# Kernel tuning notes

Measured on AMD Instinct MI355X. Metric: run time of the kernel, lower is better.

Reference implementation:

```python
import jax, jax.numpy as jnp
import numpy as np

N_ENT = 500000   # entity vocab
N_REL = 500      # relation vocab
D = 128          # embed_size
H = 256          # hidden_size
B = 4096         # number of support pairs
NBR = 32         # neighbors per node
NODES = 2 * B
T = NODES * NBR  # total neighbor edges


def setup_inputs() -> dict:
    key = jax.random.key(0)
    ks = jax.random.split(key, 12)
    entities = jax.random.randint(ks[0], (NODES,), 0, N_ENT)
    neighbor_entities = jax.random.randint(ks[1], (T,), 0, N_ENT)
    neighbor_relations = jax.random.randint(ks[2], (T,), 0, N_REL)
    offsets = (jnp.arange(NODES) * NBR).astype(jnp.int64 if jax.config.read('jax_enable_x64') else jnp.int32)
    def init(k, shape, fan_in):
        return jax.random.normal(k, shape, dtype=jnp.float32) * (1.0 / np.sqrt(fan_in))
    return dict(
        entity_embeddings=init(ks[3], (N_ENT, D), D),
        relation_embeddings=init(ks[4], (N_REL, D), D),
        Wt=init(ks[5], (D, H), D),      bt=jnp.zeros((H,), jnp.float32),
        Wn=init(ks[6], (2 * D, H), 2 * D), bn=jnp.zeros((H,), jnp.float32),
        Wr=init(ks[7], (2 * H, H), 2 * H), br=jnp.zeros((H,), jnp.float32),
        entities=entities,
        neighbor_entities=neighbor_entities,
        neighbor_relations=neighbor_relations,
        offsets=offsets,
    )


def _segment_mean(table, idx, offsets, num_segments):
    # embedding_bag(mode='mean') with ragged offsets
    n = idx.shape[0]
    seg = jnp.searchsorted(offsets, jnp.arange(n), side='right') - 1   # [T] bag id per edge
    counts = jnp.diff(jnp.concatenate([offsets, jnp.array([n], offsets.dtype)]))
    summed = jax.ops.segment_sum(table[idx], seg, num_segments=num_segments)
    return summed / jnp.maximum(counts, 1).astype(table.dtype)[:, None]


def reference(entity_embeddings, relation_embeddings, Wt, bt, Wn, bn, Wr, br,
              entities, neighbor_entities, neighbor_relations, offsets):
    nodes = entities.shape[0]
    # self-entity transform
    ent = entity_embeddings[entities] @ Wt + bt                        # [2B, H]
    # neighbor mean-aggregation (entity + relation bags share offsets)
    ne = _segment_mean(entity_embeddings, neighbor_entities, offsets, nodes)    # [2B, D]
    nr = _segment_mean(relation_embeddings, neighbor_relations, offsets, nodes)  # [2B, D]
    nbr = jnp.concatenate([ne, nr], axis=-1) @ Wn + bn                 # [2B, H]
    node = jax.nn.relu(ent + nbr).reshape(nodes // 2, 2 * Wt.shape[1])  # [B, 2H]
    pair = jax.nn.relu(node @ Wr + br)                                 # [B, H]
    return pair
```

## Files before the change

### kernel.cpp

```cpp
#include <hip/hip_runtime.h>
#include <hip/hip_bf16.h>

#define N_ENT   500000
#define N_REL   500
#define D       128
#define H       256
#define NPAIR   4096
#define NBR     32
#define NODES   8192
#define T_EDGES 262144
#define K1      384
#define K2      512

typedef __bf16  bf16x8  __attribute__((ext_vector_type(8)));
typedef float   floatx4 __attribute__((ext_vector_type(4)));

__device__ inline unsigned short f2bf(float f) {
  unsigned u = __float_as_uint(f);
  unsigned r = (u + 0x7fffu + ((u >> 16) & 1u)) >> 16;
  return (unsigned short)r;
}

__global__ __launch_bounds__(256) void gather_kernel(
    const float* __restrict__ ent_emb, const float* __restrict__ rel_emb,
    const int* __restrict__ entities, const int* __restrict__ nbr_ent,
    const int* __restrict__ nbr_rel, const int* __restrict__ offsets,
    unsigned short* __restrict__ X)
{
  int wave = threadIdx.x >> 6;
  int lane = threadIdx.x & 63;
  int n = blockIdx.x * 4 + wave;

  int beg = offsets[n];
  int end = (n + 1 < NODES) ? offsets[n + 1] : T_EDGES;
  int cnt = end - beg;

  const float2* ent2 = (const float2*)ent_emb;
  const float2* rel2 = (const float2*)rel_emb;

  int self = entities[n];
  float2 s = ent2[(long)self * 64 + lane];

  float sex = 0.f, sey = 0.f, srx = 0.f, sry = 0.f;

  if (cnt == NBR) {
    int ie[NBR], ir[NBR];
    #pragma unroll
    for (int k = 0; k < NBR; ++k) ie[k] = nbr_ent[beg + k];
    #pragma unroll
    for (int k = 0; k < NBR; ++k) ir[k] = nbr_rel[beg + k];

    #pragma unroll
    for (int c = 0; c < NBR / 8; ++c) {
      float2 e[8], r[8];
      #pragma unroll
      for (int j = 0; j < 8; ++j) e[j] = ent2[(long)ie[c * 8 + j] * 64 + lane];
      #pragma unroll
      for (int j = 0; j < 8; ++j) r[j] = rel2[(long)ir[c * 8 + j] * 64 + lane];
      #pragma unroll
      for (int j = 0; j < 8; ++j) {
        sex += e[j].x; sey += e[j].y;
        srx += r[j].x; sry += r[j].y;
      }
    }
  } else {
    for (int k = beg; k < end; ++k) {
      float2 e = ent2[(long)nbr_ent[k] * 64 + lane];
      float2 r = rel2[(long)nbr_rel[k] * 64 + lane];
      sex += e.x; sey += e.y; srx += r.x; sry += r.y;
    }
  }

  int cc = cnt < 1 ? 1 : cnt;
  float inv = 1.f / (float)cc;

  unsigned short* row = X + (long)n * K1;
  ushort2* p0 = (ushort2*)(row) + lane;
  ushort2* p1 = (ushort2*)(row + D) + lane;
  ushort2* p2 = (ushort2*)(row + 2 * D) + lane;
  *p0 = make_ushort2(f2bf(s.x), f2bf(s.y));
  *p1 = make_ushort2(f2bf(sex * inv), f2bf(sey * inv));
  *p2 = make_ushort2(f2bf(srx * inv), f2bf(sry * inv));
}

__global__ __launch_bounds__(256) void prep_weights(
    const float* __restrict__ Wt, const float* __restrict__ Wn,
    const float* __restrict__ Wr,
    unsigned short* __restrict__ W1t, unsigned short* __restrict__ W2t)
{
  int idx = blockIdx.x * 256 + threadIdx.x;
  if (idx < H * K1) {
    int nn = idx / K1, k = idx % K1;
    float v = (k < D) ? Wt[k * H + nn] : Wn[(k - D) * H + nn];
    W1t[idx] = f2bf(v);
  }
  if (idx < H * K2) {
    int nn = idx / K2, k = idx % K2;
    W2t[idx] = f2bf(Wr[k * H + nn]);
  }
}

template<int K>
__global__ __launch_bounds__(256) void gemm_bias_relu(
    const bf16x8* __restrict__ A8,
    const bf16x8* __restrict__ Bt8,
    const float* __restrict__ bias0, const float* __restrict__ bias1,
    unsigned short* __restrict__ out_bf, float* __restrict__ out_f, int N)
{
  constexpr int K8 = K / 8;
  __shared__ bf16x8 Ash[64 * 4];
  __shared__ bf16x8 Bsh[64 * 4];

  int tid  = threadIdx.x;
  int wave = tid >> 6, lane = tid & 63;
  int quad = lane >> 4, l15 = lane & 15;
  int bm = blockIdx.x * 64, bn = blockIdx.y * 64;
  int r  = tid >> 2;
  int s4 = tid & 3;

  floatx4 acc[4];
  #pragma unroll
  for (int i = 0; i < 4; ++i) acc[i] = (floatx4){0.f, 0.f, 0.f, 0.f};

  for (int k0 = 0; k0 < K8; k0 += 4) {
    Ash[tid] = A8[(long)(bm + r) * K8 + k0 + s4];
    Bsh[tid] = Bt8[(long)(bn + r) * K8 + k0 + s4];
    __syncthreads();
    bf16x8 a = Ash[(wave * 16 + l15) * 4 + quad];
    #pragma unroll
    for (int nt = 0; nt < 4; ++nt) {
      bf16x8 b = Bsh[(nt * 16 + l15) * 4 + quad];
      acc[nt] = __builtin_amdgcn_mfma_f32_16x16x32_bf16(a, b, acc[nt], 0, 0, 0);
    }
    __syncthreads();
  }

  #pragma unroll
  for (int nt = 0; nt < 4; ++nt) {
    int gn = bn + nt * 16 + l15;
    float bs = bias0[gn] + (bias1 ? bias1[gn] : 0.f);
    #pragma unroll
    for (int i = 0; i < 4; ++i) {
      long gm = bm + wave * 16 + quad * 4 + i;
      float v = acc[nt][i] + bs;
      v = v > 0.f ? v : 0.f;
      if (out_bf) out_bf[gm * N + gn] = f2bf(v);
      else        out_f [gm * N + gn] = v;
    }
  }
}

extern "C" void kernel_launch(void* const* d_in, const int* in_sizes, int n_in,
                              void* d_out, int out_size, void* d_ws, size_t ws_size,
                              hipStream_t stream) {
  const float* ent_emb = (const float*)d_in[0];
  const float* rel_emb = (const float*)d_in[1];
  const float* Wt      = (const float*)d_in[2];
  const float* bt      = (const float*)d_in[3];
  const float* Wn      = (const float*)d_in[4];
  const float* bn      = (const float*)d_in[5];
  const float* Wr      = (const float*)d_in[6];
  const float* br      = (const float*)d_in[7];
  const int* entities  = (const int*)d_in[8];
  const int* nbr_ent   = (const int*)d_in[9];
  const int* nbr_rel   = (const int*)d_in[10];
  const int* offsets   = (const int*)d_in[11];

  char* ws = (char*)d_ws;
  unsigned short* X    = (unsigned short*)(ws);
  unsigned short* node = (unsigned short*)(ws + 6291456);
  unsigned short* W1t  = (unsigned short*)(ws + 10485760);
  unsigned short* W2t  = (unsigned short*)(ws + 10682368);

  gather_kernel<<<dim3(NODES / 4), dim3(256), 0, stream>>>(
      ent_emb, rel_emb, entities, nbr_ent, nbr_rel, offsets, X);

  prep_weights<<<dim3((H * K2 + 255) / 256), dim3(256), 0, stream>>>(
      Wt, Wn, Wr, W1t, W2t);

  gemm_bias_relu<K1><<<dim3(NODES / 64, H / 64), dim3(256), 0, stream>>>(
      (const bf16x8*)X, (const bf16x8*)W1t, bt, bn,
      node, (float*)nullptr, H);

  gemm_bias_relu<K2><<<dim3(NPAIR / 64, H / 64), dim3(256), 0, stream>>>(
      (const bf16x8*)node, (const bf16x8*)W2t, br, (const float*)nullptr,
      (unsigned short*)nullptr, (float*)d_out, H);
}
```

Before: 358.3 us.

## Fuse weight prep into gather, widen gather batches, double-buffer GEMM tiles

Merges the weight transpose/convert kernel into the gather launch as extra blocks, saving one kernel launch and letting the two run at the same time. The gather now issues 16 neighbor loads per batch instead of 8 and marks the node index as wave-uniform, to keep more memory requests in flight. The GEMM now loads 64-wide K tiles into double-buffered, padded shared memory and prefetches the next tile into registers while the MFMAs run, which halves the number of barriers. These changes raise register and LDS use, which may lower occupancy.

```diff
diff --git a/kernel.cpp b/kernel.cpp
--- a/kernel.cpp
+++ b/kernel.cpp
@@ -12,6 +12,9 @@
 #define K1      384
 #define K2      512
 
+#define NB_GATHER (NODES / 4)
+#define NB_PREP   ((H * K2) / 256)
+
 typedef __bf16  bf16x8  __attribute__((ext_vector_type(8)));
 typedef float   floatx4 __attribute__((ext_vector_type(4)));
 
@@ -21,19 +24,37 @@
   return (unsigned short)r;
 }
 
-__global__ __launch_bounds__(256) void gather_kernel(
+__global__ __launch_bounds__(256) void gather_prep_kernel(
     const float* __restrict__ ent_emb, const float* __restrict__ rel_emb,
+    const float* __restrict__ Wt, const float* __restrict__ Wn,
+    const float* __restrict__ Wr,
     const int* __restrict__ entities, const int* __restrict__ nbr_ent,
     const int* __restrict__ nbr_rel, const int* __restrict__ offsets,
-    unsigned short* __restrict__ X)
+    unsigned short* __restrict__ X,
+    unsigned short* __restrict__ W1t, unsigned short* __restrict__ W2t)
 {
+  if (blockIdx.x >= NB_GATHER) {
+    int idx = (blockIdx.x - NB_GATHER) * 256 + threadIdx.x;
+    if (idx < H * K1) {
+      int nn = idx / K1, k = idx % K1;
+      float v = (k < D) ? Wt[k * H + nn] : Wn[(k - D) * H + nn];
+      W1t[idx] = f2bf(v);
+    }
+    {
+      int nn = idx / K2, k = idx % K2;
+      W2t[idx] = f2bf(Wr[k * H + nn]);
+    }
+    return;
+  }
+
   int wave = threadIdx.x >> 6;
   int lane = threadIdx.x & 63;
-  int n = blockIdx.x * 4 + wave;
+  int n = __builtin_amdgcn_readfirstlane(blockIdx.x * 4 + wave);
 
   int beg = offsets[n];
   int end = (n + 1 < NODES) ? offsets[n + 1] : T_EDGES;
   int cnt = end - beg;
+  beg = __builtin_amdgcn_readfirstlane(beg);
 
   const float2* ent2 = (const float2*)ent_emb;
   const float2* rel2 = (const float2*)rel_emb;
@@ -51,14 +72,16 @@
     for (int k = 0; k < NBR; ++k) ir[k] = nbr_rel[beg + k];
 
     #pragma unroll
-    for (int c = 0; c < NBR / 8; ++c) {
-      float2 e[8], r[8];
-      #pragma unroll
-      for (int j = 0; j < 8; ++j) e[j] = ent2[(long)ie[c * 8 + j] * 64 + lane];
-      #pragma unroll
-      for (int j = 0; j < 8; ++j) r[j] = rel2[(long)ir[c * 8 + j] * 64 + lane];
-      #pragma unroll
-      for (int j = 0; j < 8; ++j) {
+    for (int c = 0; c < 2; ++c) {
+      float2 e[16], r[16];
+      #pragma unroll
+      for (int j = 0; j < 16; ++j)
+        e[j] = ent2[(long)ie[c * 16 + j] * 64 + lane];
+      #pragma unroll
+      for (int j = 0; j < 16; ++j)
+        r[j] = rel2[(long)ir[c * 16 + j] * 64 + lane];
+      #pragma unroll
+      for (int j = 0; j < 16; ++j) {
         sex += e[j].x; sey += e[j].y;
         srx += r[j].x; sry += r[j].y;
       }
@@ -83,23 +106,6 @@
   *p2 = make_ushort2(f2bf(srx * inv), f2bf(sry * inv));
 }
 
-__global__ __launch_bounds__(256) void prep_weights(
-    const float* __restrict__ Wt, const float* __restrict__ Wn,
-    const float* __restrict__ Wr,
-    unsigned short* __restrict__ W1t, unsigned short* __restrict__ W2t)
-{
-  int idx = blockIdx.x * 256 + threadIdx.x;
-  if (idx < H * K1) {
-    int nn = idx / K1, k = idx % K1;
-    float v = (k < D) ? Wt[k * H + nn] : Wn[(k - D) * H + nn];
-    W1t[idx] = f2bf(v);
-  }
-  if (idx < H * K2) {
-    int nn = idx / K2, k = idx % K2;
-    W2t[idx] = f2bf(Wr[k * H + nn]);
-  }
-}
-
 template<int K>
 __global__ __launch_bounds__(256) void gemm_bias_relu(
     const bf16x8* __restrict__ A8,
@@ -107,32 +113,52 @@
     const float* __restrict__ bias0, const float* __restrict__ bias1,
     unsigned short* __restrict__ out_bf, float* __restrict__ out_f, int N)
 {
-  constexpr int K8 = K / 8;
-  __shared__ bf16x8 Ash[64 * 4];
-  __shared__ bf16x8 Bsh[64 * 4];
+  constexpr int K8  = K / 8;
+  constexpr int NIT = K / 64;
+  __shared__ bf16x8 sA[2][64 * 9];
+  __shared__ bf16x8 sB[2][64 * 9];
 
   int tid  = threadIdx.x;
   int wave = tid >> 6, lane = tid & 63;
   int quad = lane >> 4, l15 = lane & 15;
   int bm = blockIdx.x * 64, bn = blockIdx.y * 64;
-  int r  = tid >> 2;
-  int s4 = tid & 3;
+  int r0 = tid >> 3;
+  int u0 = tid & 7;
 
   floatx4 acc[4];
   #pragma unroll
   for (int i = 0; i < 4; ++i) acc[i] = (floatx4){0.f, 0.f, 0.f, 0.f};
 
-  for (int k0 = 0; k0 < K8; k0 += 4) {
-    Ash[tid] = A8[(long)(bm + r) * K8 + k0 + s4];
-    Bsh[tid] = Bt8[(long)(bn + r) * K8 + k0 + s4];
+  bf16x8 pa0 = A8[(long)(bm + r0) * K8 + u0];
+  bf16x8 pa1 = A8[(long)(bm + r0 + 32) * K8 + u0];
+  bf16x8 pb0 = Bt8[(long)(bn + r0) * K8 + u0];
+  bf16x8 pb1 = Bt8[(long)(bn + r0 + 32) * K8 + u0];
+  sA[0][r0 * 9 + u0] = pa0;  sA[0][(r0 + 32) * 9 + u0] = pa1;
+  sB[0][r0 * 9 + u0] = pb0;  sB[0][(r0 + 32) * 9 + u0] = pb1;
+
+  for (int it = 0; it < NIT; ++it) {
     __syncthreads();
-    bf16x8 a = Ash[(wave * 16 + l15) * 4 + quad];
-    #pragma unroll
-    for (int nt = 0; nt < 4; ++nt) {
-      bf16x8 b = Bsh[(nt * 16 + l15) * 4 + quad];
-      acc[nt] = __builtin_amdgcn_mfma_f32_16x16x32_bf16(a, b, acc[nt], 0, 0, 0);
-    }
-    __syncthreads();
+    int cur = it & 1, nxt = cur ^ 1;
+    if (it + 1 < NIT) {
+      int ko = (it + 1) * 8 + u0;
+      pa0 = A8[(long)(bm + r0) * K8 + ko];
+      pa1 = A8[(long)(bm + r0 + 32) * K8 + ko];
+      pb0 = Bt8[(long)(bn + r0) * K8 + ko];
+      pb1 = Bt8[(long)(bn + r0 + 32) * K8 + ko];
+    }
+    #pragma unroll
+    for (int kk = 0; kk < 2; ++kk) {
+      bf16x8 a = sA[cur][(wave * 16 + l15) * 9 + kk * 4 + quad];
+      #pragma unroll
+      for (int nt = 0; nt < 4; ++nt) {
+        bf16x8 b = sB[cur][(nt * 16 + l15) * 9 + kk * 4 + quad];
+        acc[nt] = __builtin_amdgcn_mfma_f32_16x16x32_bf16(a, b, acc[nt], 0, 0, 0);
+      }
+    }
+    if (it + 1 < NIT) {
+      sA[nxt][r0 * 9 + u0] = pa0;  sA[nxt][(r0 + 32) * 9 + u0] = pa1;
+      sB[nxt][r0 * 9 + u0] = pb0;  sB[nxt][(r0 + 32) * 9 + u0] = pb1;
+    }
   }
 
   #pragma unroll
@@ -172,11 +198,9 @@
   unsigned short* W1t  = (unsigned short*)(ws + 10485760);
   unsigned short* W2t  = (unsigned short*)(ws + 10682368);
 
-  gather_kernel<<<dim3(NODES / 4), dim3(256), 0, stream>>>(
-      ent_emb, rel_emb, entities, nbr_ent, nbr_rel, offsets, X);
-
-  prep_weights<<<dim3((H * K2 + 255) / 256), dim3(256), 0, stream>>>(
-      Wt, Wn, Wr, W1t, W2t);
+  gather_prep_kernel<<<dim3(NB_GATHER + NB_PREP), dim3(256), 0, stream>>>(
+      ent_emb, rel_emb, Wt, Wn, Wr,
+      entities, nbr_ent, nbr_rel, offsets, X, W1t, W2t);
 
   gemm_bias_relu<K1><<<dim3(NODES / 64, H / 64), dim3(256), 0, stream>>>(
       (const bf16x8*)X, (const bf16x8*)W1t, bt, bn,
```

After: 349.5 us. 1.03x faster.
